# Kernel tuning notes

Measured on AMD Instinct MI355X. Metric: run time of the kernel, lower is better.

## Reference

```python
import jax, jax.numpy as jnp
import numpy as np

B, L, D_INNER, D_STATE, DT_RANK = 1, 1024, 5120, 16, 160


def setup_inputs() -> dict:
    key = jax.random.key(0)
    k0, k1, k2, k3, k4, k5 = jax.random.split(key, 6)
    x = jax.random.normal(k0, (B, L, D_INNER), dtype=jnp.float32)
    # A_log in [0,1) -> A = -exp(A_log) in [-e,-1]: stable decaying recurrence
    A_log = jax.random.uniform(k1, (D_INNER, D_STATE), dtype=jnp.float32)
    D = jax.random.normal(k2, (D_INNER,), dtype=jnp.float32)
    x_proj_w = jax.random.normal(k3, (DT_RANK + 2 * D_STATE, D_INNER), dtype=jnp.float32) * 0.02
    dt_proj_w = jax.random.normal(k4, (D_INNER, DT_RANK), dtype=jnp.float32) * 0.02
    dt_proj_b = jax.random.normal(k5, (D_INNER,), dtype=jnp.float32) * 0.02
    return {"x": x, "A_log": A_log, "D": D, "x_proj_w": x_proj_w,
            "dt_proj_w": dt_proj_w, "dt_proj_b": dt_proj_b}


def reference(x, A_log, D, x_proj_w, dt_proj_w, dt_proj_b):
    # Mamba ssm(): x (b, l, d_inner) -> y (b, l, d_inner)
    A = -jnp.exp(A_log)                                   # (d, n)
    x_dbl = jnp.einsum('bld,ed->ble', x, x_proj_w)        # (b, l, dt_rank+2n)
    dt = x_dbl[..., :DT_RANK]                             # (b, l, r)
    Bm = x_dbl[..., DT_RANK:DT_RANK + D_STATE]            # (b, l, n)
    Cm = x_dbl[..., DT_RANK + D_STATE:]                   # (b, l, n)
    delta = jax.nn.softplus(jnp.einsum('blr,dr->bld', dt, dt_proj_w) + dt_proj_b)

    # discretization (zero-order hold)
    deltaA = jnp.exp(jnp.einsum('bld,dn->bldn', delta, A))        # (b, l, d, n)
    deltaB_u = jnp.einsum('bld,bln,bld->bldn', delta, Bm, x)      # (b, l, d, n)

    def step(h, inp):
        dA_t, dBu_t, c_t = inp          # (b,d,n), (b,d,n), (b,n)
        h = dA_t * h + dBu_t
        y_t = jnp.einsum('bdn,bn->bd', h, c_t)
        return h, y_t

    h0 = jnp.zeros((x.shape[0], D_INNER, D_STATE), dtype=x.dtype)
    xs = (jnp.swapaxes(deltaA, 0, 1),   # (l, b, d, n)
          jnp.swapaxes(deltaB_u, 0, 1),
          jnp.swapaxes(Cm, 0, 1))
    _, ys = jax.lax.scan(step, h0, xs)  # ys: (l, b, d)
    y = jnp.swapaxes(ys, 0, 1)          # (b, l, d)
    return y + x * D
```

## Files before the change

kernel.cpp:

```cpp
#include <hip/hip_runtime.h>
#include <hip/hip_bf16.h>

#define L_SEQ 1024
#define DI    5120
#define DS    16
#define DR    160
#define NE    192
#define NC    16
#define CL    64
#define SPLITK 16
#define KSPLIT (DI / SPLITK)
#define BK    64

#define OFF_P     0
#define SZ_P      (SPLITK * L_SEQ * NE * 4)
#define OFF_XDBL  (OFF_P + SZ_P)
#define SZ_XDBL   (L_SEQ * NE * 4)
#define OFF_DELTA (OFF_XDBL + SZ_XDBL)
#define SZ_DELTA  (L_SEQ * DI * 4)
#define OFF_HEND  (OFF_DELTA + SZ_DELTA)
#define SZ_H      (NC * DS * DI * 4)
#define OFF_APROD (OFF_HEND + SZ_H)
#define WS_END0   (OFF_APROD + SZ_H)
#define OFF_WH    OFF_HEND
#define OFF_WL    (OFF_WH + 1638400)
#define OFF_XH    (OFF_WL + 1638400)
#define OFF_XL    (OFF_XH + 393216)
#define OFF_XPH   WS_END0
#define OFF_XPL   (OFF_XPH + 10485760)
#define OFF_XWH   (OFF_XPL + 10485760)
#define OFF_XWL   (OFF_XWH + 1966080)

typedef short s16x8 __attribute__((ext_vector_type(8)));
typedef float f32x4 __attribute__((ext_vector_type(4)));

__device__ __forceinline__ unsigned short bf_rn(float f) {
  unsigned u = __float_as_uint(f);
  u += 0x7FFFu + ((u >> 16) & 1u);
  return (unsigned short)(u >> 16);
}
__device__ __forceinline__ void split_hilo(float f, unsigned short& h, unsigned short& l) {
  h = bf_rn(f);
  float hf = __uint_as_float(((unsigned)h) << 16);
  l = bf_rn(f - hf);
}

__global__ __launch_bounds__(256) void k_cvt(const float* __restrict__ src,
                                             unsigned short* __restrict__ hi,
                                             unsigned short* __restrict__ lo,
                                             int n4) {
  int i = blockIdx.x * 256 + threadIdx.x;
  if (i >= n4) return;
  int i4 = i * 4;
  float4 v = *(const float4*)&src[i4];
  float f[4] = {v.x, v.y, v.z, v.w};
  ushort4 h, l;
  unsigned short hh, ll;
  split_hilo(f[0], hh, ll); h.x = hh; l.x = ll;
  split_hilo(f[1], hh, ll); h.y = hh; l.y = ll;
  split_hilo(f[2], hh, ll); h.z = hh; l.z = ll;
  split_hilo(f[3], hh, ll); h.w = hh; l.w = ll;
  *(ushort4*)&hi[i4] = h;
  *(ushort4*)&lo[i4] = l;
}

#define AST2 72
__global__ __launch_bounds__(256) void k_xdbl_mfma2(const unsigned short* __restrict__ xph,
                                                    const unsigned short* __restrict__ xpl,
                                                    const unsigned short* __restrict__ wxh,
                                                    const unsigned short* __restrict__ wxl,
                                                    float* __restrict__ part) {
  __shared__ unsigned short sAh[64 * AST2];
  __shared__ unsigned short sAl[64 * AST2];
  const int tid  = threadIdx.x;
  const int lane = tid & 63;
  const int w    = tid >> 6;
  const int wl_  = w >> 1;
  const int we   = w & 1;
  const int l0   = blockIdx.y * 64;
  const int e0   = blockIdx.x * 64 + we * 32;
  const int kb   = blockIdx.z * KSPLIT;
  const int rc   = lane & 15;
  const int kg   = (lane >> 4) * 8;

  f32x4 acc[2][2] = {};
  for (int k0 = 0; k0 < KSPLIT; k0 += BK) {
    __syncthreads();
    for (int idx = tid; idx < 64 * 8; idx += 256) {
      int r = idx >> 3, c8 = (idx & 7) * 8;
      *(s16x8*)&sAh[r * AST2 + c8] = *(const s16x8*)&xph[(size_t)(l0 + r) * DI + kb + k0 + c8];
      *(s16x8*)&sAl[r * AST2 + c8] = *(const s16x8*)&xpl[(size_t)(l0 + r) * DI + kb + k0 + c8];
    }
    __syncthreads();
#pragma unroll
    for (int ks = 0; ks < BK; ks += 32) {
      s16x8 ah[2], al[2], bh[2], bl[2];
#pragma unroll
      for (int mf = 0; mf < 2; ++mf) {
        int row = wl_ * 32 + mf * 16 + rc;
        ah[mf] = *(const s16x8*)&sAh[row * AST2 + ks + kg];
        al[mf] = *(const s16x8*)&sAl[row * AST2 + ks + kg];
      }
#pragma unroll
      for (int nf = 0; nf < 2; ++nf) {
        size_t e = e0 + nf * 16 + rc;
        bh[nf] = *(const s16x8*)&wxh[e * DI + kb + k0 + ks + kg];
        bl[nf] = *(const s16x8*)&wxl[e * DI + kb + k0 + ks + kg];
      }
#pragma unroll
      for (int mf = 0; mf < 2; ++mf)
#pragma unroll
        for (int nf = 0; nf < 2; ++nf) {
          acc[mf][nf] = __builtin_amdgcn_mfma_f32_16x16x32_bf16(ah[mf], bh[nf], acc[mf][nf], 0, 0, 0);
          acc[mf][nf] = __builtin_amdgcn_mfma_f32_16x16x32_bf16(ah[mf], bl[nf], acc[mf][nf], 0, 0, 0);
          acc[mf][nf] = __builtin_amdgcn_mfma_f32_16x16x32_bf16(al[mf], bh[nf], acc[mf][nf], 0, 0, 0);
        }
    }
  }
#pragma unroll
  for (int mf = 0; mf < 2; ++mf)
#pragma unroll
    for (int nf = 0; nf < 2; ++nf)
#pragma unroll
      for (int r = 0; r < 4; ++r) {
        int l = l0 + wl_ * 32 + mf * 16 + (lane >> 4) * 4 + r;
        int e = e0 + nf * 16 + rc;
        part[((size_t)blockIdx.z * L_SEQ + l) * NE + e] = acc[mf][nf][r];
      }
}

__global__ __launch_bounds__(256) void k_xdbl_reduce(const float* __restrict__ part,
                                                     float* __restrict__ xdbl,
                                                     unsigned short* __restrict__ xh,
                                                     unsigned short* __restrict__ xl) {
  int i4 = (blockIdx.x * 256 + threadIdx.x) * 4;
  float4 s = {0.f, 0.f, 0.f, 0.f};
#pragma unroll
  for (int z = 0; z < SPLITK; ++z) {
    float4 p = *(const float4*)&part[(size_t)z * L_SEQ * NE + i4];
    s.x += p.x; s.y += p.y; s.z += p.z; s.w += p.w;
  }
  *(float4*)&xdbl[i4] = s;
  float f[4] = {s.x, s.y, s.z, s.w};
  ushort4 h, l;
  unsigned short hh, ll;
  split_hilo(f[0], hh, ll); h.x = hh; l.x = ll;
  split_hilo(f[1], hh, ll); h.y = hh; l.y = ll;
  split_hilo(f[2], hh, ll); h.z = hh; l.z = ll;
  split_hilo(f[3], hh, ll); h.w = hh; l.w = ll;
  *(ushort4*)&xh[i4] = h;
  *(ushort4*)&xl[i4] = l;
}

#define AST 168
__global__ __launch_bounds__(512) void k_delta_mfma2(const unsigned short* __restrict__ xh,
                                                     const unsigned short* __restrict__ xl,
                                                     const unsigned short* __restrict__ wh,
                                                     const unsigned short* __restrict__ wlo,
                                                     const float* __restrict__ dtb,
                                                     float* __restrict__ delta) {
  __shared__ unsigned short sAh[64 * AST];
  __shared__ unsigned short sAl[64 * AST];
  const int tid  = threadIdx.x;
  const int lane = tid & 63;
  const int w    = tid >> 6;
  const int wl_  = w >> 2;
  const int wd   = w & 3;
  const int l0   = blockIdx.y * 64;
  const int d0   = blockIdx.x * 128 + wd * 32;
  const int rc   = lane & 15;
  const int kg   = (lane >> 4) * 8;

  for (int idx = tid; idx < 64 * 20; idx += 512) {
    int r = idx / 20, c8 = (idx % 20) * 8;
    *(s16x8*)&sAh[r * AST + c8] = *(const s16x8*)&xh[(size_t)(l0 + r) * NE + c8];
    *(s16x8*)&sAl[r * AST + c8] = *(const s16x8*)&xl[(size_t)(l0 + r) * NE + c8];
  }
  __syncthreads();

  f32x4 acc[2][2] = {};
#pragma unroll
  for (int k0 = 0; k0 < DR; k0 += 32) {
    s16x8 ah[2], al[2], bh[2], bl[2];
#pragma unroll
    for (int mf = 0; mf < 2; ++mf) {
      int row = wl_ * 32 + mf * 16 + rc;
      ah[mf] = *(const s16x8*)&sAh[row * AST + k0 + kg];
      al[mf] = *(const s16x8*)&sAl[row * AST + k0 + kg];
    }
#pragma unroll
    for (int nf = 0; nf < 2; ++nf) {
      size_t d = d0 + nf * 16 + rc;
      bh[nf] = *(const s16x8*)&wh[d * DR + k0 + kg];
      bl[nf] = *(const s16x8*)&wlo[d * DR + k0 + kg];
    }
#pragma unroll
    for (int mf = 0; mf < 2; ++mf)
#pragma unroll
      for (int nf = 0; nf < 2; ++nf) {
        acc[mf][nf] = __builtin_amdgcn_mfma_f32_16x16x32_bf16(ah[mf], bh[nf], acc[mf][nf], 0, 0, 0);
        acc[mf][nf] = __builtin_amdgcn_mfma_f32_16x16x32_bf16(ah[mf], bl[nf], acc[mf][nf], 0, 0, 0);
        acc[mf][nf] = __builtin_amdgcn_mfma_f32_16x16x32_bf16(al[mf], bh[nf], acc[mf][nf], 0, 0, 0);
      }
  }
#pragma unroll
  for (int nf = 0; nf < 2; ++nf) {
    int d = d0 + nf * 16 + rc;
    float bias = dtb[d];
#pragma unroll
    for (int mf = 0; mf < 2; ++mf)
#pragma unroll
      for (int r = 0; r < 4; ++r) {
        int l = l0 + wl_ * 32 + mf * 16 + (lane >> 4) * 4 + r;
        float z = acc[mf][nf][r] + bias;
        float sp = fmaxf(z, 0.f) + __logf(1.f + __expf(-fabsf(z)));
        delta[(size_t)l * DI + d] = sp;
      }
  }
}

__global__ __launch_bounds__(256) void k_scan1(const float* __restrict__ x,
                                               const float* __restrict__ delta,
                                               const float* __restrict__ xdbl,
                                               const float* __restrict__ A_log,
                                               float* __restrict__ hend,
                                               float* __restrict__ aprod) {
  const int lane = threadIdx.x & 63;
  const int w    = threadIdx.x >> 6;
  const int d    = blockIdx.x * 64 + w * 16 + (lane & 15);
  const int ng   = lane >> 4;
  const int c    = blockIdx.y;
  __shared__ __align__(16) float sB[CL][DS];
  for (int i = threadIdx.x; i < CL * DS; i += 256) {
    int t = i >> 4, n = i & 15;
    sB[t][n] = xdbl[(size_t)(c * CL + t) * NE + DR + n];
  }
  __syncthreads();
  float4 av = *(const float4*)&A_log[(size_t)d * DS + ng * 4];
  float a[4] = {-__expf(av.x), -__expf(av.y), -__expf(av.z), -__expf(av.w)};
  float h[4] = {0.f, 0.f, 0.f, 0.f};
  float sdl = 0.f;

  const float* dp = &delta[(size_t)(c * CL) * DI + d];
  const float* xp = &x[(size_t)(c * CL) * DI + d];
  float dlb[8], xvb[8];
#pragma unroll
  for (int j = 0; j < 8; ++j) { dlb[j] = dp[(size_t)j * DI]; xvb[j] = xp[(size_t)j * DI]; }
  for (int tt = 0; tt < CL; tt += 8) {
#pragma unroll
    for (int j = 0; j < 8; ++j) {
      float dl = dlb[j], xv = xvb[j];
      int tn = tt + 8 + j;
      if (tn < CL) { dlb[j] = dp[(size_t)tn * DI]; xvb[j] = xp[(size_t)tn * DI]; }
      float du = dl * xv;
      sdl += dl;
      float4 b4 = *(const float4*)&sB[tt + j][ng * 4];
      float bb[4] = {b4.x, b4.y, b4.z, b4.w};
#pragma unroll
      for (int q = 0; q < 4; ++q) {
        float dA = __expf(dl * a[q]);
        h[q] = dA * h[q] + du * bb[q];
      }
    }
  }
#pragma unroll
  for (int q = 0; q < 4; ++q) {
    int n = ng * 4 + q;
    hend[(size_t)(c * DS + n) * DI + d] = h[q];
    aprod[(size_t)(c * DS + n) * DI + d] = __expf(a[q] * sdl);
  }
}

__global__ __launch_bounds__(256) void k_scan2(float* __restrict__ hend,
                                               const float* __restrict__ aprod) {
  int i = blockIdx.x * 256 + threadIdx.x;
  float ap[NC], hv[NC];
#pragma unroll
  for (int c = 0; c < NC; ++c) {
    size_t idx = (size_t)c * DS * DI + i;
    ap[c] = aprod[idx];
    hv[c] = hend[idx];
  }
  float carry = 0.f;
#pragma unroll
  for (int c = 0; c < NC; ++c) {
    size_t idx = (size_t)c * DS * DI + i;
    hend[idx] = carry;
    carry = ap[c] * carry + hv[c];
  }
}

__global__ __launch_bounds__(256) void k_scan3(const float* __restrict__ x,
                                               const float* __restrict__ delta,
                                               const float* __restrict__ xdbl,
                                               const float* __restrict__ A_log,
                                               const float* __restrict__ Dvec,
                                               const float* __restrict__ hstart,
                                               float* __restrict__ out) {
  const int lane = threadIdx.x & 63;
  const int w    = threadIdx.x >> 6;
  const int d    = blockIdx.x * 64 + w * 16 + (lane & 15);
  const int ng   = lane >> 4;
  const int c    = blockIdx.y;
  __shared__ __align__(16) float sB[CL][DS];
  __shared__ __align__(16) float sC[CL][DS];
  for (int i = threadIdx.x; i < CL * DS; i += 256) {
    int t = i >> 4, n = i & 15;
    sB[t][n] = xdbl[(size_t)(c * CL + t) * NE + DR + n];
    sC[t][n] = xdbl[(size_t)(c * CL + t) * NE + DR + DS + n];
  }
  __syncthreads();
  float4 av = *(const float4*)&A_log[(size_t)d * DS + ng * 4];
  float a[4] = {-__expf(av.x), -__expf(av.y), -__expf(av.z), -__expf(av.w)};
  float h[4];
#pragma unroll
  for (int q = 0; q < 4; ++q)
    h[q] = hstart[(size_t)(c * DS + ng * 4 + q) * DI + d];
  const float Dv = Dvec[d];

  const float* dp = &delta[(size_t)(c * CL) * DI + d];
  const float* xp = &x[(size_t)(c * CL) * DI + d];
  float* op = &out[(size_t)(c * CL) * DI + d];
  float dlb[8], xvb[8];
#pragma unroll
  for (int j = 0; j < 8; ++j) { dlb[j] = dp[(size_t)j * DI]; xvb[j] = xp[(size_t)j * DI]; }
  for (int tt = 0; tt < CL; tt += 8) {
#pragma unroll
    for (int j = 0; j < 8; ++j) {
      float dl = dlb[j], xv = xvb[j];
      int tn = tt + 8 + j;
      if (tn < CL) { dlb[j] = dp[(size_t)tn * DI]; xvb[j] = xp[(size_t)tn * DI]; }
      float du = dl * xv;
      float4 b4 = *(const float4*)&sB[tt + j][ng * 4];
      float4 c4 = *(const float4*)&sC[tt + j][ng * 4];
      float bb[4] = {b4.x, b4.y, b4.z, b4.w};
      float cc[4] = {c4.x, c4.y, c4.z, c4.w};
      float y = 0.f;
#pragma unroll
      for (int q = 0; q < 4; ++q) {
        float dA = __expf(dl * a[q]);
        h[q] = dA * h[q] + du * bb[q];
        y += h[q] * cc[q];
      }
      y += __shfl_xor(y, 16, 64);
      y += __shfl_xor(y, 32, 64);
      if (ng == 0) op[(size_t)(tt + j) * DI] = fmaf(xv, Dv, y);
    }
  }
}

extern "C" void kernel_launch(void* const* d_in, const int* in_sizes, int n_in,
                              void* d_out, int out_size, void* d_ws, size_t ws_size,
                              hipStream_t stream) {
  const float* x     = (const float*)d_in[0];
  const float* A_log = (const float*)d_in[1];
  const float* Dvec  = (const float*)d_in[2];
  const float* xw    = (const float*)d_in[3];
  const float* dtw   = (const float*)d_in[4];
  const float* dtb   = (const float*)d_in[5];
  float* out = (float*)d_out;

  char* ws = (char*)d_ws;
  float* part  = (float*)(ws + OFF_P);
  float* xdbl  = (float*)(ws + OFF_XDBL);
  float* delta = (float*)(ws + OFF_DELTA);
  float* hend  = (float*)(ws + OFF_HEND);
  float* aprod = (float*)(ws + OFF_APROD);
  unsigned short* wh  = (unsigned short*)(ws + OFF_WH);
  unsigned short* wl  = (unsigned short*)(ws + OFF_WL);
  unsigned short* xh  = (unsigned short*)(ws + OFF_XH);
  unsigned short* xl  = (unsigned short*)(ws + OFF_XL);
  unsigned short* xph = (unsigned short*)(ws + OFF_XPH);
  unsigned short* xpl = (unsigned short*)(ws + OFF_XPL);
  unsigned short* wxh = (unsigned short*)(ws + OFF_XWH);
  unsigned short* wxl = (unsigned short*)(ws + OFF_XWL);

  k_cvt<<<5120, 256, 0, stream>>>(x, xph, xpl, L_SEQ * DI / 4);
  k_cvt<<<960, 256, 0, stream>>>(xw, wxh, wxl, NE * DI / 4);
  k_cvt<<<800, 256, 0, stream>>>(dtw, wh, wl, DI * DR / 4);
  k_xdbl_mfma2<<<dim3(3, 16, SPLITK), 256, 0, stream>>>(xph, xpl, wxh, wxl, part);
  k_xdbl_reduce<<<192, 256, 0, stream>>>(part, xdbl, xh, xl);
  k_delta_mfma2<<<dim3(40, 16), 512, 0, stream>>>(xh, xl, wh, wl, dtb, delta);
  k_scan1<<<dim3(80, NC), 256, 0, stream>>>(x, delta, xdbl, A_log, hend, aprod);
  k_scan2<<<320, 256, 0, stream>>>(hend, aprod);
  k_scan3<<<dim3(80, NC), 256, 0, stream>>>(x, delta, xdbl, A_log, Dvec, hend, out);
}
```

Measured before the change: 107.2 us.

## Halve scan chunk length, use exp2 with prescaled A, stage outputs through LDS

Cuts the scan chunk length from 64 to 32 and doubles the chunk count, so the chunked scan kernels have twice as many blocks and each block runs a shorter serial recurrence. It also rewrites the workspace offsets to make room for the larger per-chunk state buffers. The decay exponent now uses exp2f with A premultiplied by log2(e), dropping a multiply per exponential. In the final scan kernel, outputs are collected in shared memory and written as coalesced float4 rows instead of scattered scalar stores. The tradeoff is twice as much chunk-boundary state traffic and a longer carry pass in the second scan kernel.

After: 121.6 us. +13.4%, slower.

```diff
diff --git a/kernel.cpp b/kernel.cpp
--- a/kernel.cpp
+++ b/kernel.cpp
@@ -6,30 +6,26 @@
 #define DS    16
 #define DR    160
 #define NE    192
-#define NC    16
-#define CL    64
+#define NC    32
+#define CL    32
 #define SPLITK 16
 #define KSPLIT (DI / SPLITK)
 #define BK    64
+#define LOG2E 1.44269504088896340736f
 
 #define OFF_P     0
-#define SZ_P      (SPLITK * L_SEQ * NE * 4)
-#define OFF_XDBL  (OFF_P + SZ_P)
-#define SZ_XDBL   (L_SEQ * NE * 4)
-#define OFF_DELTA (OFF_XDBL + SZ_XDBL)
-#define SZ_DELTA  (L_SEQ * DI * 4)
-#define OFF_HEND  (OFF_DELTA + SZ_DELTA)
-#define SZ_H      (NC * DS * DI * 4)
-#define OFF_APROD (OFF_HEND + SZ_H)
-#define WS_END0   (OFF_APROD + SZ_H)
-#define OFF_WH    OFF_HEND
-#define OFF_WL    (OFF_WH + 1638400)
-#define OFF_XH    (OFF_WL + 1638400)
-#define OFF_XL    (OFF_XH + 393216)
-#define OFF_XPH   WS_END0
-#define OFF_XPL   (OFF_XPH + 10485760)
-#define OFF_XWH   (OFF_XPL + 10485760)
-#define OFF_XWL   (OFF_XWH + 1966080)
+#define OFF_XDBL  12582912
+#define OFF_WH    13369344
+#define OFF_WL    15007744
+#define OFF_XH    16646144
+#define OFF_XL    17039360
+#define OFF_XPH   17432576
+#define OFF_XPL   27918336
+#define OFF_XWH   38404096
+#define OFF_XWL   40370176
+#define OFF_DELTA 42336256
+#define OFF_HEND  63307776
+#define OFF_APROD 73793536
 
 typedef short s16x8 __attribute__((ext_vector_type(8)));
 typedef float f32x4 __attribute__((ext_vector_type(4)));
@@ -237,7 +233,8 @@
   }
   __syncthreads();
   float4 av = *(const float4*)&A_log[(size_t)d * DS + ng * 4];
-  float a[4] = {-__expf(av.x), -__expf(av.y), -__expf(av.z), -__expf(av.w)};
+  float aL[4] = {-__expf(av.x) * LOG2E, -__expf(av.y) * LOG2E,
+                 -__expf(av.z) * LOG2E, -__expf(av.w) * LOG2E};
   float h[4] = {0.f, 0.f, 0.f, 0.f};
   float sdl = 0.f;
 
@@ -258,7 +255,7 @@
       float bb[4] = {b4.x, b4.y, b4.z, b4.w};
 #pragma unroll
       for (int q = 0; q < 4; ++q) {
-        float dA = __expf(dl * a[q]);
+        float dA = exp2f(dl * aL[q]);
         h[q] = dA * h[q] + du * bb[q];
       }
     }
@@ -267,7 +264,7 @@
   for (int q = 0; q < 4; ++q) {
     int n = ng * 4 + q;
     hend[(size_t)(c * DS + n) * DI + d] = h[q];
-    aprod[(size_t)(c * DS + n) * DI + d] = __expf(a[q] * sdl);
+    aprod[(size_t)(c * DS + n) * DI + d] = exp2f(aL[q] * sdl);
   }
 }
 
@@ -297,21 +294,24 @@
                                                const float* __restrict__ Dvec,
                                                const float* __restrict__ hstart,
                                                float* __restrict__ out) {
-  const int lane = threadIdx.x & 63;
-  const int w    = threadIdx.x >> 6;
+  const int tid  = threadIdx.x;
+  const int lane = tid & 63;
+  const int w    = tid >> 6;
   const int d    = blockIdx.x * 64 + w * 16 + (lane & 15);
   const int ng   = lane >> 4;
   const int c    = blockIdx.y;
   __shared__ __align__(16) float sB[CL][DS];
   __shared__ __align__(16) float sC[CL][DS];
-  for (int i = threadIdx.x; i < CL * DS; i += 256) {
+  __shared__ __align__(16) float sY[CL][64];
+  for (int i = tid; i < CL * DS; i += 256) {
     int t = i >> 4, n = i & 15;
     sB[t][n] = xdbl[(size_t)(c * CL + t) * NE + DR + n];
     sC[t][n] = xdbl[(size_t)(c * CL + t) * NE + DR + DS + n];
   }
   __syncthreads();
   float4 av = *(const float4*)&A_log[(size_t)d * DS + ng * 4];
-  float a[4] = {-__expf(av.x), -__expf(av.y), -__expf(av.z), -__expf(av.w)};
+  float aL[4] = {-__expf(av.x) * LOG2E, -__expf(av.y) * LOG2E,
+                 -__expf(av.z) * LOG2E, -__expf(av.w) * LOG2E};
   float h[4];
 #pragma unroll
   for (int q = 0; q < 4; ++q)
@@ -320,7 +320,6 @@
 
   const float* dp = &delta[(size_t)(c * CL) * DI + d];
   const float* xp = &x[(size_t)(c * CL) * DI + d];
-  float* op = &out[(size_t)(c * CL) * DI + d];
   float dlb[8], xvb[8];
 #pragma unroll
   for (int j = 0; j < 8; ++j) { dlb[j] = dp[(size_t)j * DI]; xvb[j] = xp[(size_t)j * DI]; }
@@ -338,14 +337,20 @@
       float y = 0.f;
 #pragma unroll
       for (int q = 0; q < 4; ++q) {
-        float dA = __expf(dl * a[q]);
+        float dA = exp2f(dl * aL[q]);
         h[q] = dA * h[q] + du * bb[q];
         y += h[q] * cc[q];
       }
       y += __shfl_xor(y, 16, 64);
       y += __shfl_xor(y, 32, 64);
-      if (ng == 0) op[(size_t)(tt + j) * DI] = fmaf(xv, Dv, y);
-    }
+      if (ng == 0) sY[tt + j][w * 16 + (lane & 15)] = fmaf(xv, Dv, y);
+    }
+  }
+  __syncthreads();
+  for (int i = tid; i < CL * 16; i += 256) {
+    int t = i >> 4, seg = i & 15;
+    float4 v = *(const float4*)&sY[t][seg * 4];
+    *(float4*)&out[(size_t)(c * CL + t) * DI + blockIdx.x * 64 + seg * 4] = v;
   }
 }
 
```
